# Performance work log

Measured on AMD Instinct MI355X. Metric: run time of the kernel, lower is better.

The kernel has to match this reference:

```python
import jax, jax.numpy as jnp
import numpy as np

B, L, F, D = 128, 64, 3072, 1024
CV, CN = 512, 1024  # verb/noun concept channels
MAX_K = (L + 7) // 8
BN_EPS = 1e-5


def setup_inputs() -> dict:
    key = jax.random.key(0)
    ks = jax.random.split(key, 24)
    s_in = 1.0 / np.sqrt(F)
    s_d = 1.0 / np.sqrt(D)
    inp = {
        'inputs': jax.random.normal(ks[0], (B, L, F), jnp.float32),
        'input_lens': jax.random.randint(ks[1], (B,), 1, L + 1, jnp.int32),
        # three level linear embeds
        'W0': jax.random.normal(ks[2], (F, D), jnp.float32) * s_in,
        'b0': jnp.zeros((D,), jnp.float32),
        'W1': jax.random.normal(ks[3], (F, D), jnp.float32) * s_in,
        'b1': jnp.zeros((D,), jnp.float32),
        'W2': jax.random.normal(ks[4], (F, D), jnp.float32) * s_in,
        'b2': jnp.zeros((D,), jnp.float32),
        # attention scorer
        'w_attn': jax.random.normal(ks[5], (D, 1), jnp.float32) * s_d,
        'b_attn': jnp.zeros((1,), jnp.float32),
        # verb classifier: Conv1d(D, CV, 3, pad=1) + BN + sigmoid
        'Kv': jax.random.normal(ks[6], (CV, D, 3), jnp.float32) * (1.0 / np.sqrt(D * 3)),
        'bv': jnp.zeros((CV,), jnp.float32),
        'g_v': jnp.ones((CV,), jnp.float32),
        'beta_v': jnp.zeros((CV,), jnp.float32),
        'mean_v': jax.random.normal(ks[7], (CV,), jnp.float32) * 0.1,
        'var_v': jax.random.uniform(ks[8], (CV,), jnp.float32, 0.5, 1.5),
        # noun classifier: Conv1d(D, CN, 1) + BN + sigmoid
        'Kn': jax.random.normal(ks[9], (CN, D, 1), jnp.float32) * s_d,
        'bn_b': jnp.zeros((CN,), jnp.float32),
        'g_n': jnp.ones((CN,), jnp.float32),
        'beta_n': jnp.zeros((CN,), jnp.float32),
        'mean_n': jax.random.normal(ks[10], (CN,), jnp.float32) * 0.1,
        'var_n': jax.random.uniform(ks[11], (CN,), jnp.float32, 0.5, 1.5),
    }
    return inp


def _conv_bn_sigmoid(x_bld, K, b, gamma, beta, mean, var, pad):
    # x_bld: (B, L, D) -> permute to NCH (B, D, L) as in torch
    x = jnp.transpose(x_bld, (0, 2, 1))
    y = jax.lax.conv_general_dilated(
        x, K, window_strides=(1,), padding=[(pad, pad)],
        dimension_numbers=('NCH', 'OIH', 'NCH'))
    y = y + b[None, :, None]
    # BatchNorm1d in eval mode (running stats)
    y = (y - mean[None, :, None]) * jax.lax.rsqrt(var + BN_EPS)[None, :, None]
    y = y * gamma[None, :, None] + beta[None, :, None]
    y = jax.nn.sigmoid(y)
    return jnp.transpose(y, (0, 2, 1))  # (B, L, C)


def _topk_mean(logits, input_lens):
    # logits: (B, L, C); per-sample top-ceil(len/8) over time, then mean
    lens = input_lens.astype(jnp.int32)
    kk = (lens + 7) // 8  # (B,)
    valid = (jnp.arange(L)[None, :] < lens[:, None])  # (B, L)
    masked = jnp.where(valid[:, :, None], logits, -1e18)
    # top MAX_K per (batch, class) over time
    top = jax.lax.top_k(jnp.transpose(masked, (0, 2, 1)), MAX_K)[0]  # (B, C, MAX_K)
    take = (jnp.arange(MAX_K)[None, None, :] < kk[:, None, None]).astype(logits.dtype)
    return jnp.sum(top * take, axis=-1) / kk[:, None].astype(logits.dtype)  # (B, C)


def reference(inputs, input_lens, W0, b0, W1, b1, W2, b2, w_attn, b_attn,
              Kv, bv, g_v, beta_v, mean_v, var_v,
              Kn, bn_b, g_n, beta_n, mean_n, var_n):
    # level embeds (dropout is identity in eval)
    e0 = inputs @ W0 + b0
    e1 = inputs @ W1 + b1
    e2 = inputs @ W2 + b2

    # masked softmax attention pooling over time -> sent_embeds
    scores = (e0 @ w_attn)[:, :, 0] + b_attn[0]  # (B, L)
    valid = jnp.arange(L)[None, :] < input_lens[:, None]
    scores = jnp.where(valid, scores, -1e18)
    attn = jax.nn.softmax(scores, axis=1)
    sent_embeds = jnp.sum(e0 * attn[:, :, None], axis=1)  # (B, D)

    logits_verb = _conv_bn_sigmoid(e1, Kv, bv, g_v, beta_v, mean_v, var_v, pad=1)  # (B, L, CV)
    logits_noun = _conv_bn_sigmoid(e2, Kn, bn_b, g_n, beta_n, mean_n, var_n, pad=0)  # (B, L, CN)

    instance_logits_verb = _topk_mean(logits_verb, input_lens)  # (B, CV)
    instance_logits_noun = _topk_mean(logits_noun, input_lens)  # (B, CN)

    return (sent_embeds, e1, e2, instance_logits_verb, instance_logits_noun)
```

## Files before the change

### kernel.cpp

```cpp
#include <hip/hip_runtime.h>
#include <cstdint>
#include <cstddef>

typedef unsigned short u16;
typedef __attribute__((ext_vector_type(8))) short short8;
typedef __attribute__((ext_vector_type(4))) float f32x4;

static __device__ __forceinline__ float bf2f(u16 h) {
  union { unsigned u; float f; } a; a.u = ((unsigned)h) << 16; return a.f;
}
static __device__ __forceinline__ u16 f2bf(float x) {
  union { float f; unsigned u; } a; a.f = x;
  return (u16)((a.u + 0x7fffu + ((a.u >> 16) & 1u)) >> 16);
}

#define GLDS16(gp, lp)                                                          \
  __builtin_amdgcn_global_load_lds(                                             \
      (const __attribute__((address_space(1))) void*)(gp),                      \
      (__attribute__((address_space(3))) void*)(lp), 16, 0, 0)

__global__ void prep_all(const float* __restrict__ inputs, u16* __restrict__ Xbf,
                         const float* __restrict__ W0, const float* __restrict__ W1,
                         const float* __restrict__ W2, u16* __restrict__ Wt,
                         const float* __restrict__ Kv, const float* __restrict__ bv,
                         const float* __restrict__ g_v, const float* __restrict__ beta_v,
                         const float* __restrict__ mean_v, const float* __restrict__ var_v,
                         u16* __restrict__ KVt, float* __restrict__ biasv,
                         const float* __restrict__ Kn, const float* __restrict__ bnb,
                         const float* __restrict__ g_n, const float* __restrict__ beta_n,
                         const float* __restrict__ mean_n, const float* __restrict__ var_n,
                         u16* __restrict__ KNt, float* __restrict__ biasn,
                         u16* __restrict__ e1pad) {
  __shared__ float tile[32][33];
  const int id = blockIdx.x;
  const int tid = threadIdx.x;
  if (id < 24576) {
    const int i = id * 256 + tid;
    float4 v = ((const float4*)inputs)[i];
    ushort4 o;
    o.x = f2bf(v.x); o.y = f2bf(v.y); o.z = f2bf(v.z); o.w = f2bf(v.w);
    ((ushort4*)Xbf)[i] = o;
  } else if (id < 33792) {
    const int idd = id - 24576;
    const int kb = (idd % 96) * 32;
    const int jb = (idd / 96) * 32;
    const int tx = tid & 31, ty = tid >> 5;
    const int w = jb >> 10;
    const float* W = (w == 0) ? W0 : ((w == 1) ? W1 : W2);
    const int nb = jb & 1023;
    for (int i = ty; i < 32; i += 8)
      tile[i][tx] = W[(size_t)(kb + i) * 1024 + nb + tx];
    __syncthreads();
    for (int i = ty; i < 32; i += 8)
      Wt[(size_t)(jb + i) * 3072 + kb + tx] = f2bf(tile[tx][i]);
  } else if (id < 34304) {
    const int c = id - 33792;
    const float scale = g_v[c] * rsqrtf(var_v[c] + 1e-5f);
    for (int t = 0; t < 3; t++)
      for (int d = tid; d < 1024; d += 256)
        KVt[(size_t)c * 3072 + t * 1024 + d] = f2bf(Kv[(size_t)c * 3072 + d * 3 + t] * scale);
    if (tid == 0) biasv[c] = (bv[c] - mean_v[c]) * scale + beta_v[c];
  } else if (id < 35328) {
    const int c = id - 34304;
    const float scale = g_n[c] * rsqrtf(var_n[c] + 1e-5f);
    for (int d = tid; d < 1024; d += 256)
      KNt[(size_t)c * 1024 + d] = f2bf(Kn[(size_t)c * 1024 + d] * scale);
    if (tid == 0) biasn[c] = (bnb[c] - mean_n[c]) * scale + beta_n[c];
  } else {
    const int i = (id - 35328) * 256 + tid;
    const int b = i >> 11;
    const int j = i & 2047;
    const int r = (j < 1024) ? 0 : 65;
    const int d = j & 1023;
    e1pad[(size_t)(b * 66 + r) * 1024 + d] = 0;
  }
}

#define SLOT 24576

#define MFMA16_()                                                                  \
  acc[0][0] = __builtin_amdgcn_mfma_f32_16x16x32_bf16(a0, b0, acc[0][0], 0, 0, 0); \
  acc[0][1] = __builtin_amdgcn_mfma_f32_16x16x32_bf16(a0, b1, acc[0][1], 0, 0, 0); \
  acc[0][2] = __builtin_amdgcn_mfma_f32_16x16x32_bf16(a0, b2, acc[0][2], 0, 0, 0); \
  acc[0][3] = __builtin_amdgcn_mfma_f32_16x16x32_bf16(a0, b3, acc[0][3], 0, 0, 0); \
  acc[1][0] = __builtin_amdgcn_mfma_f32_16x16x32_bf16(a1, b0, acc[1][0], 0, 0, 0); \
  acc[1][1] = __builtin_amdgcn_mfma_f32_16x16x32_bf16(a1, b1, acc[1][1], 0, 0, 0); \
  acc[1][2] = __builtin_amdgcn_mfma_f32_16x16x32_bf16(a1, b2, acc[1][2], 0, 0, 0); \
  acc[1][3] = __builtin_amdgcn_mfma_f32_16x16x32_bf16(a1, b3, acc[1][3], 0, 0, 0); \
  acc[2][0] = __builtin_amdgcn_mfma_f32_16x16x32_bf16(a2, b0, acc[2][0], 0, 0, 0); \
  acc[2][1] = __builtin_amdgcn_mfma_f32_16x16x32_bf16(a2, b1, acc[2][1], 0, 0, 0); \
  acc[2][2] = __builtin_amdgcn_mfma_f32_16x16x32_bf16(a2, b2, acc[2][2], 0, 0, 0); \
  acc[2][3] = __builtin_amdgcn_mfma_f32_16x16x32_bf16(a2, b3, acc[2][3], 0, 0, 0); \
  acc[3][0] = __builtin_amdgcn_mfma_f32_16x16x32_bf16(a3, b0, acc[3][0], 0, 0, 0); \
  acc[3][1] = __builtin_amdgcn_mfma_f32_16x16x32_bf16(a3, b1, acc[3][1], 0, 0, 0); \
  acc[3][2] = __builtin_amdgcn_mfma_f32_16x16x32_bf16(a3, b2, acc[3][2], 0, 0, 0); \
  acc[3][3] = __builtin_amdgcn_mfma_f32_16x16x32_bf16(a3, b3, acc[3][3], 0, 0, 0);

#define KTILE_(CUR, NXT, T)                                                     \
  {                                                                             \
    const int t_ = (T);                                                         \
    const bool st_ = (t_ + 2 < NT);                                             \
    const size_t kk_ = (size_t)(t_ + 2) * 64;                                   \
    {                                                      \
      const u16* ra = rdA + (CUR) * SLOT;                                       \
      const u16* rb = rdB + (CUR) * SLOT;                                       \
      short8 a0 = *(const short8*)(ra + p0);                                    \
      short8 a1 = *(const short8*)(ra + 1024 + p0);                             \
      short8 a2 = *(const short8*)(ra + 2048 + p0);                             \
      short8 a3 = *(const short8*)(ra + 3072 + p0);                             \
      short8 b0 = *(const short8*)(rb + p0);                                    \
      short8 b1 = *(const short8*)(rb + 1024 + p0);                             \
      short8 b2 = *(const short8*)(rb + 2048 + p0);                             \
      short8 b3 = *(const short8*)(rb + 3072 + p0);                             \
      if (st_) {                                                                \
        GLDS16(gA + kk_, stA + (NXT) * SLOT);                                   \
        GLDS16(gA + hA + kk_, stA + (NXT) * SLOT + 4096);                       \
        GLDS16(gB + kk_, stB + (NXT) * SLOT);                                   \
      }                                                                         \
      __builtin_amdgcn_s_barrier();                                             \
      asm volatile("s_waitcnt lgkmcnt(0)" ::: "memory");                        \
      __builtin_amdgcn_s_setprio(1);                                            \
      MFMA16_();                                                                \
      __builtin_amdgcn_s_setprio(0);                                            \
      __builtin_amdgcn_s_barrier();                                             \
    }                                                                           \
    {                                                      \
      const u16* ra = rdA + (CUR) * SLOT;                                       \
      const u16* rb = rdB + (CUR) * SLOT;                                       \
      short8 a0 = *(const short8*)(ra + p1);                                    \
      short8 a1 = *(const short8*)(ra + 1024 + p1);                             \
      short8 a2 = *(const short8*)(ra + 2048 + p1);                             \
      short8 a3 = *(const short8*)(ra + 3072 + p1);                             \
      short8 b0 = *(const short8*)(rb + p1);                                    \
      short8 b1 = *(const short8*)(rb + 1024 + p1);                             \
      short8 b2 = *(const short8*)(rb + 2048 + p1);                             \
      short8 b3 = *(const short8*)(rb + 3072 + p1);                             \
      if (st_) {                                                                \
        GLDS16(gB + hB + kk_, stB + (NXT) * SLOT + 4096);                       \
        GLDS16(gB + 2 * hB + kk_, stB + (NXT) * SLOT + 8192);                   \
        GLDS16(gB + 3 * hB + kk_, stB + (NXT) * SLOT + 12288);                  \
      }                                                                         \
      __builtin_amdgcn_s_barrier();                                             \
      asm volatile("s_waitcnt lgkmcnt(0)" ::: "memory");                        \
      __builtin_amdgcn_s_setprio(1);                                            \
      MFMA16_();                                                                \
      __builtin_amdgcn_s_setprio(0);                                            \
      if (t_ < NT - 2) {                                                        \
        asm volatile("s_waitcnt vmcnt(6)" ::: "memory");                        \
      } else if (t_ == NT - 2) {                                                \
        asm volatile("s_waitcnt vmcnt(0)" ::: "memory");                        \
      }                                                                         \
      __builtin_amdgcn_s_barrier();                                             \
    }                                                                           \
  }

template<int NT>
static __device__ __forceinline__ void gemm_pipe(
    const u16* __restrict__ gA, const size_t hA,
    const u16* __restrict__ gB, const size_t hB,
    u16* lds, f32x4 (&acc)[4][4]) {
  const int tid = threadIdx.x;
  const int lane = tid & 63;
  const int warp = tid >> 6;
  const int wm = warp & 1, wn = warp >> 1;
  const int l15 = lane & 15, quad = lane >> 4;

  u16* stA = lds + tid * 8;
  u16* stB = lds + 8192 + tid * 8;
  const u16* rdA = lds + (wm * 64 + l15) * 64;
  const u16* rdB = lds + 8192 + (wn * 64 + l15) * 64;
  const int p0 = ((quad + l15) & 7) * 8;
  const int p1 = p0 ^ 32;

#pragma unroll
  for (int s = 0; s < 2; s++) {
    const size_t kk = (size_t)s * 64;
    GLDS16(gA + kk, stA + s * SLOT);
    GLDS16(gA + hA + kk, stA + s * SLOT + 4096);
    GLDS16(gB + kk, stB + s * SLOT);
    GLDS16(gB + hB + kk, stB + s * SLOT + 4096);
    GLDS16(gB + 2 * hB + kk, stB + s * SLOT + 8192);
    GLDS16(gB + 3 * hB + kk, stB + s * SLOT + 12288);
  }
  asm volatile("s_waitcnt vmcnt(6)" ::: "memory");
  __builtin_amdgcn_s_barrier();

#pragma unroll 1
  for (int t = 0; t < NT; t += 3) {
    KTILE_(0, 2, t);
    if (t + 1 < NT) KTILE_(1, 0, t + 1);
    if (t + 2 < NT) KTILE_(2, 1, t + 2);
  }
}

static __device__ __forceinline__ void topk_epilogue(
    f32x4 (&acc)[4][4], const float* __restrict__ bias,
    const int* __restrict__ lens, float* __restrict__ out,
    const int NC, const int m0, const int n0) {
  const int tid = threadIdx.x;
  const int lane = tid & 63;
  const int warp = tid >> 6;
  const int wm = warp & 1, wn = warp >> 1;
  const int l15 = lane & 15, quad = lane >> 4;
  const int b = (m0 >> 6) + wm;
  const int len = lens[b];
  const int kk8 = (len + 7) >> 3;
#pragma unroll
  for (int j = 0; j < 4; j++) {
    const int c = n0 + wn * 64 + j * 16 + l15;
    const float bias_c = bias[c];
    float t[8];
#pragma unroll
    for (int q8 = 0; q8 < 8; q8++) t[q8] = -1e30f;
#pragma unroll
    for (int i = 0; i < 4; i++) {
#pragma unroll
      for (int r = 0; r < 4; r++) {
        const int l = i * 16 + quad * 4 + r;
        const float v = acc[i][j][r] + bias_c;
        const float sg = 1.0f / (1.0f + __expf(-v));
        float x = (l < len) ? sg : -1e30f;
#pragma unroll
        for (int q8 = 0; q8 < 8; q8++) {
          const float hi = fmaxf(t[q8], x);
          x = fminf(t[q8], x);
          t[q8] = hi;
        }
      }
    }
#pragma unroll
    for (int mask = 16; mask <= 32; mask <<= 1) {
      float xs[8];
#pragma unroll
      for (int q8 = 0; q8 < 8; q8++) xs[q8] = __shfl_xor(t[q8], mask);
#pragma unroll
      for (int q8 = 0; q8 < 8; q8++) {
        float x = xs[q8];
#pragma unroll
        for (int p8 = 0; p8 < 8; p8++) {
          const float hi = fmaxf(t[p8], x);
          x = fminf(t[p8], x);
          t[p8] = hi;
        }
      }
    }
    if (quad == 0) {
      float s = 0.f;
#pragma unroll
      for (int q8 = 0; q8 < 8; q8++) s += (q8 < kk8) ? t[q8] : 0.f;
      out[(size_t)b * NC + c] = s / (float)kk8;
    }
  }
}

__global__ __launch_bounds__(512, 2) void gemm_embed(
    const u16* __restrict__ A, const u16* __restrict__ Bmat,
    const float* __restrict__ bias0, const float* __restrict__ bias1,
    const float* __restrict__ bias2,
    float* __restrict__ oute1, float* __restrict__ oute2,
    u16* __restrict__ e0bf, u16* __restrict__ e1pad, u16* __restrict__ e2bf) {
  __shared__ __align__(16) u16 lds[3 * SLOT];
  const int tid = threadIdx.x;
  const int m0 = blockIdx.y * 128;
  const int n0 = blockIdx.x * 256;
  const int u = tid >> 3;
  const int c8 = (((tid & 7) - u) & 7) * 8;

  f32x4 acc[4][4];
#pragma unroll
  for (int i = 0; i < 4; i++)
#pragma unroll
    for (int j = 0; j < 4; j++) acc[i][j] = (f32x4){0.f, 0.f, 0.f, 0.f};

  gemm_pipe<48>(A + (size_t)(m0 + u) * 3072 + c8, (size_t)64 * 3072,
                Bmat + (size_t)(n0 + u) * 3072 + c8, (size_t)64 * 3072,
                lds, acc);

  const int lane = tid & 63;
  const int warp = tid >> 6;
  const int wm = warp & 1, wn = warp >> 1;
  const int l15 = lane & 15, quad = lane >> 4;
  const int w = n0 >> 10;
  const float* bp = (w == 0) ? bias0 : ((w == 1) ? bias1 : bias2);
#pragma unroll
  for (int i = 0; i < 4; i++) {
    const int mrow = m0 + wm * 64 + i * 16 + quad * 4;
#pragma unroll
    for (int j = 0; j < 4; j++) {
      const int c = n0 + wn * 64 + j * 16 + l15;
      const int n = c & 1023;
      const float bias = bp[n];
#pragma unroll
      for (int r = 0; r < 4; r++) {
        const int m = mrow + r;
        const float v = acc[i][j][r] + bias;
        if (w == 0) {
          e0bf[(size_t)m * 1024 + n] = f2bf(v);
        } else if (w == 1) {
          oute1[(size_t)m * 1024 + n] = v;
          const int bb = m >> 6, ll = m & 63;
          e1pad[(size_t)(bb * 66 + ll + 1) * 1024 + n] = f2bf(v);
        } else {
          oute2[(size_t)m * 1024 + n] = v;
          e2bf[(size_t)m * 1024 + n] = f2bf(v);
        }
      }
    }
  }
}

__global__ __launch_bounds__(512, 2) void fused_tail(
    const u16* __restrict__ e1pad, const u16* __restrict__ KVt,
    const float* __restrict__ biasv,
    const u16* __restrict__ e2bf, const u16* __restrict__ KNt,
    const float* __restrict__ biasn,
    const u16* __restrict__ e0bf, const float* __restrict__ w_attn,
    const float* __restrict__ b_attn, const int* __restrict__ lens,
    float* __restrict__ out_sent, float* __restrict__ out_ilv,
    float* __restrict__ out_iln) {
  __shared__ __align__(16) u16 smem[3 * SLOT];
  const int id = blockIdx.x;
  const int tid = threadIdx.x;
  if (id < 384) {
    const int u = tid >> 3;
    const int c8 = (((tid & 7) - u) & 7) * 8;
    f32x4 acc[4][4];
#pragma unroll
    for (int i = 0; i < 4; i++)
#pragma unroll
      for (int j = 0; j < 4; j++) acc[i][j] = (f32x4){0.f, 0.f, 0.f, 0.f};
    if (id < 128) {
      const int by = id >> 1, bx = id & 1;
      const int n0 = bx * 256;
      gemm_pipe<48>(e1pad + ((size_t)(by * 2) * 66 + u) * 1024 + c8, (size_t)66 * 1024,
                    KVt + (size_t)(n0 + u) * 3072 + c8, (size_t)64 * 3072,
                    smem, acc);
      topk_epilogue(acc, biasv, lens, out_ilv, 512, by * 128, n0);
    } else {
      const int id2 = id - 128;
      const int by = id2 >> 2, bx = id2 & 3;
      const int m0 = by * 128, n0 = bx * 256;
      gemm_pipe<16>(e2bf + (size_t)(m0 + u) * 1024 + c8, (size_t)64 * 1024,
                    KNt + (size_t)(n0 + u) * 1024 + c8, (size_t)64 * 1024,
                    smem, acc);
      topk_epilogue(acc, biasn, lens, out_iln, 1024, m0, n0);
    }
  } else {
    const int b = id - 384;
    const int lane = tid & 63;
    const int warp = tid >> 6;
    float* sc = (float*)smem;
    float* at = sc + 64;
    const int len = lens[b];
    if (warp < 4) {
      for (int t = 0; t < 16; t++) {
        const int l = warp * 16 + t;
        const u16* row = e0bf + (size_t)(b * 64 + l) * 1024;
        float s = 0.f;
#pragma unroll
        for (int uu = 0; uu < 16; uu++) {
          const int d = lane + uu * 64;
          s += bf2f(row[d]) * w_attn[d];
        }
#pragma unroll
        for (int off = 32; off > 0; off >>= 1) s += __shfl_down(s, off);
        if (lane == 0) sc[l] = s + b_attn[0];
      }
    }
    __syncthreads();
    if (warp == 0) {
      float v = (lane < len) ? sc[lane] : -1e30f;
      float m = v;
#pragma unroll
      for (int off = 32; off > 0; off >>= 1) m = fmaxf(m, __shfl_xor(m, off));
      float p = (lane < len) ? __expf(v - m) : 0.f;
      float ssum = p;
#pragma unroll
      for (int off = 32; off > 0; off >>= 1) ssum += __shfl_xor(ssum, off);
      at[lane] = p / ssum;
    }
    __syncthreads();
    if (tid < 256) {
      const int d0 = tid * 4;
      float a0 = 0.f, a1 = 0.f, a2 = 0.f, a3 = 0.f;
      for (int l = 0; l < 64; l++) {
        const float wgt = at[l];
        const ushort4 u4 = *(const ushort4*)(e0bf + (size_t)(b * 64 + l) * 1024 + d0);
        a0 += wgt * bf2f(u4.x);
        a1 += wgt * bf2f(u4.y);
        a2 += wgt * bf2f(u4.z);
        a3 += wgt * bf2f(u4.w);
      }
      float4 o; o.x = a0; o.y = a1; o.z = a2; o.w = a3;
      *(float4*)(out_sent + (size_t)b * 1024 + d0) = o;
    }
  }
}

extern "C" void kernel_launch(void* const* d_in, const int* in_sizes, int n_in,
                              void* d_out, int out_size, void* d_ws, size_t ws_size,
                              hipStream_t stream) {
  const float* inputs = (const float*)d_in[0];
  const int*   lens   = (const int*)d_in[1];
  const float* W0 = (const float*)d_in[2];
  const float* b0 = (const float*)d_in[3];
  const float* W1 = (const float*)d_in[4];
  const float* b1 = (const float*)d_in[5];
  const float* W2 = (const float*)d_in[6];
  const float* b2 = (const float*)d_in[7];
  const float* w_attn = (const float*)d_in[8];
  const float* b_attn = (const float*)d_in[9];
  const float* Kv   = (const float*)d_in[10];
  const float* bv   = (const float*)d_in[11];
  const float* g_v  = (const float*)d_in[12];
  const float* beta_v = (const float*)d_in[13];
  const float* mean_v = (const float*)d_in[14];
  const float* var_v  = (const float*)d_in[15];
  const float* Kn   = (const float*)d_in[16];
  const float* bn_b = (const float*)d_in[17];
  const float* g_n  = (const float*)d_in[18];
  const float* beta_n = (const float*)d_in[19];
  const float* mean_n = (const float*)d_in[20];
  const float* var_n  = (const float*)d_in[21];

  float* out = (float*)d_out;
  float* out_sent = out;
  float* out_e1   = out + 131072;
  float* out_e2   = out + 131072 + 8388608;
  float* out_ilv  = out + 131072 + 2 * 8388608;
  float* out_iln  = out_ilv + 65536;

  char* p = (char*)d_ws;
  u16* Xbf  = (u16*)p; p += (size_t)8192 * 3072 * 2;
  u16* Wt   = (u16*)p; p += (size_t)3072 * 3072 * 2;
  u16* KVt  = (u16*)p; p += (size_t)512 * 3072 * 2;
  u16* KNt  = (u16*)p; p += (size_t)1024 * 1024 * 2;
  float* biasv = (float*)p; p += 512 * 4;
  float* biasn = (float*)p; p += 1024 * 4;
  u16* e0bf  = (u16*)p; p += (size_t)8192 * 1024 * 2;
  u16* e1pad = (u16*)p; p += (size_t)128 * 66 * 1024 * 2;
  u16* e2bf  = (u16*)p; p += (size_t)8192 * 1024 * 2;

  prep_all<<<36352, 256, 0, stream>>>(inputs, Xbf, W0, W1, W2, Wt,
                                      Kv, bv, g_v, beta_v, mean_v, var_v, KVt, biasv,
                                      Kn, bn_b, g_n, beta_n, mean_n, var_n, KNt, biasn,
                                      e1pad);
  gemm_embed<<<dim3(12, 64), 512, 0, stream>>>(Xbf, Wt, b0, b1, b2, out_e1, out_e2,
                                               e0bf, e1pad, e2bf);
  fused_tail<<<512, 512, 0, stream>>>(e1pad, KVt, biasv, e2bf, KNt, biasn,
                                      e0bf, w_attn, b_attn, lens,
                                      out_sent, out_ilv, out_iln);
}
```

Baseline: 453.2 us.

## Widen embed GEMM tile to 128x384 with 4-stage K=32 pipeline, batch prep blocks

The embed GEMM tile grows from 128x256 to 128x384 (6 N-fragments per warp) and the grid shrinks from 12x64 to 8x64 blocks. The shared GEMM pipeline moves from a 3-slot K=64 design with two half-steps per tile to a templated 4-slot K=32 pipeline with 3-deep prefetch and explicit vmcnt waits. The tail GEMMs use the same pipeline, and the verb GEMM adds a row offset that skips the padding rows. The prep kernel now runs far fewer blocks, each looping over 12 conversion or transpose tiles. The larger tile is meant to improve operand reuse and cut launch overhead, in exchange for more registers and LDS per block, a smaller grid, and finer K steps with more barriers.

```diff
diff --git a/kernel.cpp b/kernel.cpp
--- a/kernel.cpp
+++ b/kernel.cpp
@@ -18,6 +18,14 @@
   __builtin_amdgcn_global_load_lds(                                             \
       (const __attribute__((address_space(1))) void*)(gp),                      \
       (__attribute__((address_space(3))) void*)(lp), 16, 0, 0)
+
+template<int N> static __device__ __forceinline__ void vmwait() {
+  if constexpr (N == 0)      asm volatile("s_waitcnt vmcnt(0)" ::: "memory");
+  else if constexpr (N == 3) asm volatile("s_waitcnt vmcnt(3)" ::: "memory");
+  else if constexpr (N == 4) asm volatile("s_waitcnt vmcnt(4)" ::: "memory");
+  else if constexpr (N == 6) asm volatile("s_waitcnt vmcnt(6)" ::: "memory");
+  else if constexpr (N == 8) asm volatile("s_waitcnt vmcnt(8)" ::: "memory");
+}
 
 __global__ void prep_all(const float* __restrict__ inputs, u16* __restrict__ Xbf,
                          const float* __restrict__ W0, const float* __restrict__ W1,
@@ -34,40 +42,49 @@
   __shared__ float tile[32][33];
   const int id = blockIdx.x;
   const int tid = threadIdx.x;
-  if (id < 24576) {
-    const int i = id * 256 + tid;
-    float4 v = ((const float4*)inputs)[i];
-    ushort4 o;
-    o.x = f2bf(v.x); o.y = f2bf(v.y); o.z = f2bf(v.z); o.w = f2bf(v.w);
-    ((ushort4*)Xbf)[i] = o;
-  } else if (id < 33792) {
-    const int idd = id - 24576;
-    const int kb = (idd % 96) * 32;
-    const int jb = (idd / 96) * 32;
+  if (id < 2048) {
+    int i = id * 256 + tid;
+#pragma unroll
+    for (int it = 0; it < 12; it++) {
+      float4 v = ((const float4*)inputs)[i];
+      ushort4 o;
+      o.x = f2bf(v.x); o.y = f2bf(v.y); o.z = f2bf(v.z); o.w = f2bf(v.w);
+      ((ushort4*)Xbf)[i] = o;
+      i += 2048 * 256;
+    }
+  } else if (id < 2816) {
     const int tx = tid & 31, ty = tid >> 5;
-    const int w = jb >> 10;
-    const float* W = (w == 0) ? W0 : ((w == 1) ? W1 : W2);
-    const int nb = jb & 1023;
-    for (int i = ty; i < 32; i += 8)
-      tile[i][tx] = W[(size_t)(kb + i) * 1024 + nb + tx];
-    __syncthreads();
-    for (int i = ty; i < 32; i += 8)
-      Wt[(size_t)(jb + i) * 3072 + kb + tx] = f2bf(tile[tx][i]);
-  } else if (id < 34304) {
-    const int c = id - 33792;
+    for (int it = 0; it < 12; it++) {
+      const int tl = (id - 2048) + 768 * it;
+      const int kb = (tl % 96) * 32;
+      const int jb = (tl / 96) * 32;
+      const int w = jb >> 10;
+      const float* W = (w == 0) ? W0 : ((w == 1) ? W1 : W2);
+      const int nb = jb & 1023;
+#pragma unroll
+      for (int i = 0; i < 4; i++)
+        tile[ty + 8 * i][tx] = W[(size_t)(kb + ty + 8 * i) * 1024 + nb + tx];
+      __syncthreads();
+#pragma unroll
+      for (int i = 0; i < 4; i++)
+        Wt[(size_t)(jb + ty + 8 * i) * 3072 + kb + tx] = f2bf(tile[tx][ty + 8 * i]);
+      __syncthreads();
+    }
+  } else if (id < 3328) {
+    const int c = id - 2816;
     const float scale = g_v[c] * rsqrtf(var_v[c] + 1e-5f);
     for (int t = 0; t < 3; t++)
       for (int d = tid; d < 1024; d += 256)
         KVt[(size_t)c * 3072 + t * 1024 + d] = f2bf(Kv[(size_t)c * 3072 + d * 3 + t] * scale);
     if (tid == 0) biasv[c] = (bv[c] - mean_v[c]) * scale + beta_v[c];
-  } else if (id < 35328) {
-    const int c = id - 34304;
+  } else if (id < 4352) {
+    const int c = id - 3328;
     const float scale = g_n[c] * rsqrtf(var_n[c] + 1e-5f);
     for (int d = tid; d < 1024; d += 256)
       KNt[(size_t)c * 1024 + d] = f2bf(Kn[(size_t)c * 1024 + d] * scale);
     if (tid == 0) biasn[c] = (bnb[c] - mean_n[c]) * scale + beta_n[c];
   } else {
-    const int i = (id - 35328) * 256 + tid;
+    const int i = (id - 4352) * 256 + tid;
     const int b = i >> 11;
     const int j = i & 2047;
     const int r = (j < 1024) ? 0 : 65;
@@ -76,125 +93,85 @@
   }
 }
 
-#define SLOT 24576
-
-#define MFMA16_()                                                                  \
-  acc[0][0] = __builtin_amdgcn_mfma_f32_16x16x32_bf16(a0, b0, acc[0][0], 0, 0, 0); \
-  acc[0][1] = __builtin_amdgcn_mfma_f32_16x16x32_bf16(a0, b1, acc[0][1], 0, 0, 0); \
-  acc[0][2] = __builtin_amdgcn_mfma_f32_16x16x32_bf16(a0, b2, acc[0][2], 0, 0, 0); \
-  acc[0][3] = __builtin_amdgcn_mfma_f32_16x16x32_bf16(a0, b3, acc[0][3], 0, 0, 0); \
-  acc[1][0] = __builtin_amdgcn_mfma_f32_16x16x32_bf16(a1, b0, acc[1][0], 0, 0, 0); \
-  acc[1][1] = __builtin_amdgcn_mfma_f32_16x16x32_bf16(a1, b1, acc[1][1], 0, 0, 0); \
-  acc[1][2] = __builtin_amdgcn_mfma_f32_16x16x32_bf16(a1, b2, acc[1][2], 0, 0, 0); \
-  acc[1][3] = __builtin_amdgcn_mfma_f32_16x16x32_bf16(a1, b3, acc[1][3], 0, 0, 0); \
-  acc[2][0] = __builtin_amdgcn_mfma_f32_16x16x32_bf16(a2, b0, acc[2][0], 0, 0, 0); \
-  acc[2][1] = __builtin_amdgcn_mfma_f32_16x16x32_bf16(a2, b1, acc[2][1], 0, 0, 0); \
-  acc[2][2] = __builtin_amdgcn_mfma_f32_16x16x32_bf16(a2, b2, acc[2][2], 0, 0, 0); \
-  acc[2][3] = __builtin_amdgcn_mfma_f32_16x16x32_bf16(a2, b3, acc[2][3], 0, 0, 0); \
-  acc[3][0] = __builtin_amdgcn_mfma_f32_16x16x32_bf16(a3, b0, acc[3][0], 0, 0, 0); \
-  acc[3][1] = __builtin_amdgcn_mfma_f32_16x16x32_bf16(a3, b1, acc[3][1], 0, 0, 0); \
-  acc[3][2] = __builtin_amdgcn_mfma_f32_16x16x32_bf16(a3, b2, acc[3][2], 0, 0, 0); \
-  acc[3][3] = __builtin_amdgcn_mfma_f32_16x16x32_bf16(a3, b3, acc[3][3], 0, 0, 0);
-
-#define KTILE_(CUR, NXT, T)                                                     \
+#define PIPE_DECLS(FJv)                                                         \
+  constexpr int FJ = (FJv);                                                     \
+  constexpr int SLOTU = 4096 + FJ * 2048;                                       \
+  constexpr int NBG = FJ / 2;                                                   \
+  constexpr int G = 1 + NBG;                                                    \
+  const int tid = threadIdx.x;                                                  \
+  const int lane = tid & 63;                                                    \
+  const int warp = tid >> 6;                                                    \
+  const int wm = warp & 1, wn = warp >> 1;                                      \
+  const int l15 = lane & 15, quad = lane >> 4;                                  \
+  u16* stA = lds + tid * 8;                                                     \
+  u16* stB = lds + 4096 + tid * 8;                                              \
+  const u16* rdA = lds + (wm * 64 + l15) * 32;                                  \
+  const u16* rdB = lds + 4096 + (wn * (FJ * 16) + l15) * 32;                    \
+  const int pA = ((quad + l15) & 3) * 8;
+
+#define STAGE_(NSL, KO)                                                         \
   {                                                                             \
-    const int t_ = (T);                                                         \
-    const bool st_ = (t_ + 2 < NT);                                             \
-    const size_t kk_ = (size_t)(t_ + 2) * 64;                                   \
-    {                                                      \
-      const u16* ra = rdA + (CUR) * SLOT;                                       \
-      const u16* rb = rdB + (CUR) * SLOT;                                       \
-      short8 a0 = *(const short8*)(ra + p0);                                    \
-      short8 a1 = *(const short8*)(ra + 1024 + p0);                             \
-      short8 a2 = *(const short8*)(ra + 2048 + p0);                             \
-      short8 a3 = *(const short8*)(ra + 3072 + p0);                             \
-      short8 b0 = *(const short8*)(rb + p0);                                    \
-      short8 b1 = *(const short8*)(rb + 1024 + p0);                             \
-      short8 b2 = *(const short8*)(rb + 2048 + p0);                             \
-      short8 b3 = *(const short8*)(rb + 3072 + p0);                             \
-      if (st_) {                                                                \
-        GLDS16(gA + kk_, stA + (NXT) * SLOT);                                   \
-        GLDS16(gA + hA + kk_, stA + (NXT) * SLOT + 4096);                       \
-        GLDS16(gB + kk_, stB + (NXT) * SLOT);                                   \
-      }                                                                         \
-      __builtin_amdgcn_s_barrier();                                             \
-      asm volatile("s_waitcnt lgkmcnt(0)" ::: "memory");                        \
-      __builtin_amdgcn_s_setprio(1);                                            \
-      MFMA16_();                                                                \
-      __builtin_amdgcn_s_setprio(0);                                            \
-      __builtin_amdgcn_s_barrier();                                             \
-    }                                                                           \
-    {                                                      \
-      const u16* ra = rdA + (CUR) * SLOT;                                       \
-      const u16* rb = rdB + (CUR) * SLOT;                                       \
-      short8 a0 = *(const short8*)(ra + p1);                                    \
-      short8 a1 = *(const short8*)(ra + 1024 + p1);                             \
-      short8 a2 = *(const short8*)(ra + 2048 + p1);                             \
-      short8 a3 = *(const short8*)(ra + 3072 + p1);                             \
-      short8 b0 = *(const short8*)(rb + p1);                                    \
-      short8 b1 = *(const short8*)(rb + 1024 + p1);                             \
-      short8 b2 = *(const short8*)(rb + 2048 + p1);                             \
-      short8 b3 = *(const short8*)(rb + 3072 + p1);                             \
-      if (st_) {                                                                \
-        GLDS16(gB + hB + kk_, stB + (NXT) * SLOT + 4096);                       \
-        GLDS16(gB + 2 * hB + kk_, stB + (NXT) * SLOT + 8192);                   \
-        GLDS16(gB + 3 * hB + kk_, stB + (NXT) * SLOT + 12288);                  \
-      }                                                                         \
-      __builtin_amdgcn_s_barrier();                                             \
-      asm volatile("s_waitcnt lgkmcnt(0)" ::: "memory");                        \
-      __builtin_amdgcn_s_setprio(1);                                            \
-      MFMA16_();                                                                \
-      __builtin_amdgcn_s_setprio(0);                                            \
-      if (t_ < NT - 2) {                                                        \
-        asm volatile("s_waitcnt vmcnt(6)" ::: "memory");                        \
-      } else if (t_ == NT - 2) {                                                \
-        asm volatile("s_waitcnt vmcnt(0)" ::: "memory");                        \
-      }                                                                         \
-      __builtin_amdgcn_s_barrier();                                             \
-    }                                                                           \
-  }
-
-template<int NT>
+    const size_t ko_ = (KO);                                                    \
+    GLDS16(gA + ko_, stA + (NSL) * SLOTU);                                      \
+    _Pragma("unroll")                                                           \
+    for (int g = 0; g < NBG; g++)                                               \
+      GLDS16(gB + (size_t)g * gBgrp + ko_, stB + (NSL) * SLOTU + g * 4096);     \
+  }
+
+#define BODY_(SL, NSL, T, DOSTAGE, VM)                                          \
+  {                                                                             \
+    const u16* ra = rdA + (SL) * SLOTU + pA;                                    \
+    const u16* rb = rdB + (SL) * SLOTU + pA;                                    \
+    short8 fa[4];                                                               \
+    short8 fb[FJ];                                                              \
+    _Pragma("unroll")                                                           \
+    for (int i = 0; i < 4; i++) fa[i] = *(const short8*)(ra + i * 512);         \
+    _Pragma("unroll")                                                           \
+    for (int j = 0; j < FJ; j++) fb[j] = *(const short8*)(rb + j * 512);        \
+    if (DOSTAGE) STAGE_(NSL, (size_t)((T) + 3) * 32);                           \
+    __builtin_amdgcn_sched_barrier(0);                                          \
+    __builtin_amdgcn_s_setprio(1);                                              \
+    _Pragma("unroll")                                                           \
+    for (int i = 0; i < 4; i++)                                                 \
+      _Pragma("unroll")                                                         \
+      for (int j = 0; j < FJ; j++)                                              \
+        acc[i][j] = __builtin_amdgcn_mfma_f32_16x16x32_bf16(fa[i], fb[j],       \
+                                                            acc[i][j], 0, 0, 0);\
+    __builtin_amdgcn_s_setprio(0);                                              \
+    vmwait<VM>();                                                               \
+    __builtin_amdgcn_s_barrier();                                               \
+    __builtin_amdgcn_sched_barrier(0);                                          \
+  }
+
+template<int FJv, int NT>
 static __device__ __forceinline__ void gemm_pipe(
-    const u16* __restrict__ gA, const size_t hA,
-    const u16* __restrict__ gB, const size_t hB,
-    u16* lds, f32x4 (&acc)[4][4]) {
-  const int tid = threadIdx.x;
-  const int lane = tid & 63;
-  const int warp = tid >> 6;
-  const int wm = warp & 1, wn = warp >> 1;
-  const int l15 = lane & 15, quad = lane >> 4;
-
-  u16* stA = lds + tid * 8;
-  u16* stB = lds + 8192 + tid * 8;
-  const u16* rdA = lds + (wm * 64 + l15) * 64;
-  const u16* rdB = lds + 8192 + (wn * 64 + l15) * 64;
-  const int p0 = ((quad + l15) & 7) * 8;
-  const int p1 = p0 ^ 32;
-
-#pragma unroll
-  for (int s = 0; s < 2; s++) {
-    const size_t kk = (size_t)s * 64;
-    GLDS16(gA + kk, stA + s * SLOT);
-    GLDS16(gA + hA + kk, stA + s * SLOT + 4096);
-    GLDS16(gB + kk, stB + s * SLOT);
-    GLDS16(gB + hB + kk, stB + s * SLOT + 4096);
-    GLDS16(gB + 2 * hB + kk, stB + s * SLOT + 8192);
-    GLDS16(gB + 3 * hB + kk, stB + s * SLOT + 12288);
-  }
-  asm volatile("s_waitcnt vmcnt(6)" ::: "memory");
+    const u16* __restrict__ gA, const u16* __restrict__ gB, const size_t gBgrp,
+    u16* lds, f32x4 (*acc)[FJv]) {
+  PIPE_DECLS(FJv)
+
+  STAGE_(0, 0);
+  STAGE_(1, 32);
+  STAGE_(2, 64);
+  vmwait<2 * G>();
   __builtin_amdgcn_s_barrier();
-
+  __builtin_amdgcn_sched_barrier(0);
+
+  int t = 0;
 #pragma unroll 1
-  for (int t = 0; t < NT; t += 3) {
-    KTILE_(0, 2, t);
-    if (t + 1 < NT) KTILE_(1, 0, t + 1);
-    if (t + 2 < NT) KTILE_(2, 1, t + 2);
-  }
+  for (; t < NT - 4; t += 4) {
+    BODY_(0, 3, t,     true, 2 * G);
+    BODY_(1, 0, t + 1, true, 2 * G);
+    BODY_(2, 1, t + 2, true, 2 * G);
+    BODY_(3, 2, t + 3, true, 2 * G);
+  }
+  BODY_(0, 3, t,     true,  2 * G);
+  BODY_(1, 0, t + 1, false, G);
+  BODY_(2, 1, t + 2, false, 0);
+  BODY_(3, 2, t + 3, false, 63);
 }
 
 static __device__ __forceinline__ void topk_epilogue(
-    f32x4 (&acc)[4][4], const float* __restrict__ bias,
+    f32x4 (*acc)[4], const float* __restrict__ bias,
     const int* __restrict__ lens, float* __restrict__ out,
     const int NC, const int m0, const int n0) {
   const int tid = threadIdx.x;
@@ -259,47 +236,45 @@
     const float* __restrict__ bias2,
     float* __restrict__ oute1, float* __restrict__ oute2,
     u16* __restrict__ e0bf, u16* __restrict__ e1pad, u16* __restrict__ e2bf) {
-  __shared__ __align__(16) u16 lds[3 * SLOT];
+  __shared__ __align__(16) u16 lds[4 * (4096 + 6 * 2048)];
   const int tid = threadIdx.x;
   const int m0 = blockIdx.y * 128;
-  const int n0 = blockIdx.x * 256;
-  const int u = tid >> 3;
-  const int c8 = (((tid & 7) - u) & 7) * 8;
-
-  f32x4 acc[4][4];
+  const int n0 = blockIdx.x * 384;
+  const int u = tid >> 2;
+  const int cs = (((tid & 3) - u) & 3) * 8;
+
+  f32x4 acc[4][6];
 #pragma unroll
   for (int i = 0; i < 4; i++)
 #pragma unroll
-    for (int j = 0; j < 4; j++) acc[i][j] = (f32x4){0.f, 0.f, 0.f, 0.f};
-
-  gemm_pipe<48>(A + (size_t)(m0 + u) * 3072 + c8, (size_t)64 * 3072,
-                Bmat + (size_t)(n0 + u) * 3072 + c8, (size_t)64 * 3072,
-                lds, acc);
+    for (int j = 0; j < 6; j++) acc[i][j] = (f32x4){0.f, 0.f, 0.f, 0.f};
+
+  gemm_pipe<6, 96>(A + (size_t)(m0 + u) * 3072 + cs,
+                   Bmat + (size_t)(n0 + u) * 3072 + cs, (size_t)128 * 3072,
+                   lds, acc);
 
   const int lane = tid & 63;
   const int warp = tid >> 6;
   const int wm = warp & 1, wn = warp >> 1;
   const int l15 = lane & 15, quad = lane >> 4;
-  const int w = n0 >> 10;
-  const float* bp = (w == 0) ? bias0 : ((w == 1) ? bias1 : bias2);
-#pragma unroll
-  for (int i = 0; i < 4; i++) {
-    const int mrow = m0 + wm * 64 + i * 16 + quad * 4;
-#pragma unroll
-    for (int j = 0; j < 4; j++) {
-      const int c = n0 + wn * 64 + j * 16 + l15;
-      const int n = c & 1023;
-      const float bias = bp[n];
+#pragma unroll
+  for (int j = 0; j < 6; j++) {
+    const int cb = n0 + wn * 96 + j * 16;
+    const int w = cb >> 10;
+    const int n = (cb & 1023) + l15;
+    const float bias = ((w == 0) ? bias0 : (w == 1) ? bias1 : bias2)[n];
+#pragma unroll
+    for (int i = 0; i < 4; i++) {
+      const int mr = m0 + wm * 64 + i * 16 + quad * 4;
 #pragma unroll
       for (int r = 0; r < 4; r++) {
-        const int m = mrow + r;
+        const int m = mr + r;
         const float v = acc[i][j][r] + bias;
         if (w == 0) {
           e0bf[(size_t)m * 1024 + n] = f2bf(v);
         } else if (w == 1) {
           oute1[(size_t)m * 1024 + n] = v;
-          const int bb = m >> 6, ll = m & 63;
-          e1pad[(size_t)(bb * 66 + ll + 1) * 1024 + n] = f2bf(v);
+          e1pad[(size_t)((m >> 6) * 66 + (m & 63) + 1) * 1024 + n] = f2bf(v);
         } else {
           oute2[(size_t)m * 1024 + n] = v;
           e2bf[(size_t)m * 1024 + n] = f2bf(v);
@@ -318,12 +293,12 @@
     const float* __restrict__ b_attn, const int* __restrict__ lens,
     float* __restrict__ out_sent, float* __restrict__ out_ilv,
     float* __restrict__ out_iln) {
-  __shared__ __align__(16) u16 smem[3 * SLOT];
+  __shared__ __align__(16) u16 smem[4 * (4096 + 4 * 2048)];
   const int id = blockIdx.x;
   const int tid = threadIdx.x;
   if (id < 384) {
-    const int u = tid >> 3;
-    const int c8 = (((tid & 7) - u) & 7) * 8;
+    const int u = tid >> 2;
+    const int cs = (((tid & 3) - u) & 3) * 8;
     f32x4 acc[4][4];
 #pragma unroll
     for (int i = 0; i < 4; i++)
@@ -332,17 +307,18 @@
     if (id < 128) {
       const int by = id >> 1, bx = id & 1;
       const int n0 = bx * 256;
-      gemm_pipe<48>(e1pad + ((size_t)(by * 2) * 66 + u) * 1024 + c8, (size_t)66 * 1024,
-                    KVt + (size_t)(n0 + u) * 3072 + c8, (size_t)64 * 3072,
-                    smem, acc);
+      const int rowoff = (u < 64) ? u : (u + 2);
+      gemm_pipe<4, 96>(e1pad + ((size_t)(by * 2) * 66 + rowoff) * 1024 + cs,
+                       KVt + (size_t)(n0 + u) * 3072 + cs, (size_t)128 * 3072,
+                       smem, acc);
       topk_epilogue(acc, biasv, lens, out_ilv, 512, by * 128, n0);
     } else {
       const int id2 = id - 128;
       const int by = id2 >> 2, bx = id2 & 3;
       const int m0 = by * 128, n0 = bx * 256;
-      gemm_pipe<16>(e2bf + (size_t)(m0 + u) * 1024 + c8, (size_t)64 * 1024,
-                    KNt + (size_t)(n0 + u) * 1024 + c8, (size_t)64 * 1024,
-                    smem, acc);
+      gemm_pipe<4, 32>(e2bf + (size_t)(m0 + u) * 1024 + cs,
+                       KNt + (size_t)(n0 + u) * 1024 + cs, (size_t)128 * 1024,
+                       smem, acc);
       topk_epilogue(acc, biasn, lens, out_iln, 1024, m0, n0);
     }
   } else {
@@ -441,12 +417,12 @@
   u16* e1pad = (u16*)p; p += (size_t)128 * 66 * 1024 * 2;
   u16* e2bf  = (u16*)p; p += (size_t)8192 * 1024 * 2;
 
-  prep_all<<<36352, 256, 0, stream>>>(inputs, Xbf, W0, W1, W2, Wt,
-                                      Kv, bv, g_v, beta_v, mean_v, var_v, KVt, biasv,
-                                      Kn, bn_b, g_n, beta_n, mean_n, var_n, KNt, biasn,
-                                      e1pad);
-  gemm_embed<<<dim3(12, 64), 512, 0, stream>>>(Xbf, Wt, b0, b1, b2, out_e1, out_e2,
-                                               e0bf, e1pad, e2bf);
+  prep_all<<<5376, 256, 0, stream>>>(inputs, Xbf, W0, W1, W2, Wt,
+                                     Kv, bv, g_v, beta_v, mean_v, var_v, KVt, biasv,
+                                     Kn, bn_b, g_n, beta_n, mean_n, var_n, KNt, biasn,
+                                     e1pad);
+  gemm_embed<<<dim3(8, 64), 512, 0, stream>>>(Xbf, Wt, b0, b1, b2, out_e1, out_e2,
+                                              e0bf, e1pad, e2bf);
   fused_tail<<<512, 512, 0, stream>>>(e1pad, KVt, biasv, e2bf, KNt, biasn,
                                       e0bf, w_attn, b_attn, lens,
                                       out_sent, out_ilv, out_iln);
```

After: 490.9 us. 8.3% more time.
